# Performance work log

Hardware: AMD Instinct MI355X
Metric: run time of the kernel (lower is better)

Reference implementation:

```python
import jax, jax.numpy as jnp
import numpy as np

B, OBS, GENC, H, C, NF = 16384, 512, 216, 1024, 64, 8
IN = GENC + OBS + OBS  # use_state=True: [graph, state, next_state]


def setup_inputs() -> dict:
    key = jax.random.key(0)
    ks = jax.random.split(key, 9)
    graph = jax.random.randint(ks[0], (B, GENC), 0, 2).astype(jnp.float32)
    state = jax.random.normal(ks[1], (B, OBS), dtype=jnp.float32)
    next_state = jax.random.normal(ks[2], (B, OBS), dtype=jnp.float32)
    W1 = jax.random.normal(ks[3], (NF, IN, H), dtype=jnp.float32) * 0.02
    b1 = jnp.zeros((NF, H), dtype=jnp.float32)
    W2 = jax.random.normal(ks[4], (NF, H, H), dtype=jnp.float32) * 0.02
    b2 = jnp.zeros((NF, H), dtype=jnp.float32)
    W3 = jax.random.normal(ks[5], (NF, H, C), dtype=jnp.float32) * 0.02
    b3 = jnp.zeros((NF, C), dtype=jnp.float32)
    return {"graph": graph, "state": state, "next_state": next_state,
            "W1": W1, "b1": b1, "W2": W2, "b2": b2, "W3": W3, "b3": b3}


def reference(graph, state, next_state, W1, b1, W2, b2, W3, b3):
    # wide_diayn forward: concat input, run per-factor MLP on rows where
    # graph[:, i] == 1, later factors overwrite earlier; unmatched rows -> 0.
    x = jnp.concatenate([graph, state, next_state], axis=-1)  # [B, IN]
    nf = W1.shape[0]
    mask = graph[:, :nf] == 1.0  # [B, F] per-factor indicator
    h = jax.nn.relu(jnp.einsum('bi,fih->bfh', x, W1) + b1[None, :, :])
    h = jax.nn.relu(jnp.einsum('bfh,fhg->bfg', h, W2) + b2[None, :, :])
    out_all = jnp.einsum('bfg,fgc->bfc', h, W3) + b3[None, :, :]  # [B, F, C]
    rev_first = jnp.argmax(mask[:, ::-1].astype(jnp.int32), axis=1)
    last_idx = (nf - 1) - rev_first  # [B]
    sel = jnp.take_along_axis(out_all, last_idx[:, None, None], axis=1)[:, 0, :]
    any_active = mask.any(axis=1)
    return jnp.where(any_active[:, None], sel, jnp.zeros_like(sel))
```

## Files before the change

### kernel.cpp

```cpp
#include <hip/hip_runtime.h>

#define BB   16384
#define GENC 216
#define OBS  512
#define NH   1024
#define NC   64
#define NFAC 8
#define NIN  1240
#define KP1  1280
#define MTILES 136

typedef __attribute__((ext_vector_type(4))) float f32x4;
typedef __attribute__((ext_vector_type(8))) short short8;
typedef __attribute__((ext_vector_type(4))) short short4v;

__device__ __forceinline__ unsigned short f2bf(float f) {
  union { float f; unsigned u; } x; x.f = f;
  unsigned r = x.u + 0x7fffu + ((x.u >> 16) & 1u);
  return (unsigned short)(r >> 16);
}

__device__ __forceinline__ void gl_lds16(const unsigned short* g, unsigned short* l) {
  __builtin_amdgcn_global_load_lds(
      (const __attribute__((address_space(1))) void*)g,
      (__attribute__((address_space(3))) void*)l, 16, 0, 0);
}

__device__ __forceinline__ int xcd_chunk(int gid, int nwg) {
  int q = nwg >> 3, r = nwg & 7, x = gid & 7, p = gid >> 3;
  return (x < r ? x * (q + 1) : r * (q + 1) + (x - r) * q) + p;
}

__global__ void bucket_kernel(const float* __restrict__ graph,
                              int* __restrict__ cnt, int* __restrict__ rowlist) {
  __shared__ int lcnt[NFAC];
  __shared__ int lbase[NFAC];
  int tid = threadIdx.x;
  if (tid < NFAC) lcnt[tid] = 0;
  __syncthreads();
  int b = blockIdx.x * 256 + tid;
  const float* g = graph + (size_t)b * GENC;
  float4 g0 = *(const float4*)g;
  float4 g1 = *(const float4*)(g + 4);
  int f = -1;
  if (g0.x == 1.f) f = 0;
  if (g0.y == 1.f) f = 1;
  if (g0.z == 1.f) f = 2;
  if (g0.w == 1.f) f = 3;
  if (g1.x == 1.f) f = 4;
  if (g1.y == 1.f) f = 5;
  if (g1.z == 1.f) f = 6;
  if (g1.w == 1.f) f = 7;
  int li = 0;
  if (f >= 0) li = atomicAdd(&lcnt[f], 1);
  __syncthreads();
  if (tid < NFAC) lbase[tid] = lcnt[tid] ? atomicAdd(&cnt[tid], lcnt[tid]) : 0;
  __syncthreads();
  if (f >= 0) rowlist[f * BB + lbase[f] + li] = b;
}

__global__ void gather_x(const float* __restrict__ graph,
                         const float* __restrict__ state,
                         const float* __restrict__ nexts,
                         const int* __restrict__ cnt,
                         const int* __restrict__ rowlist,
                         unsigned short* __restrict__ xg) {
  int w = threadIdx.x >> 6, lane = threadIdx.x & 63;
  int pos = blockIdx.x * 4 + w;
  int f = -1, loc = 0, acc = 0;
#pragma unroll
  for (int i = 0; i < NFAC; ++i) {
    int c = cnt[i];
    if (f < 0 && pos < acc + c) { f = i; loc = pos - acc; }
    acc += c;
  }
  if (f < 0) return;
  int b = rowlist[f * BB + loc];
  unsigned short* dst = xg + (size_t)pos * KP1;
#pragma unroll
  for (int it = 0; it < 5; ++it) {
    int c = it * 64 + lane;
    float4 v;
    if (c < 54)       v = *(const float4*)(graph + (size_t)b * GENC + c * 4);
    else if (c < 182) v = *(const float4*)(state + (size_t)b * OBS + (c - 54) * 4);
    else if (c < 310) v = *(const float4*)(nexts + (size_t)b * OBS + (c - 182) * 4);
    else              v = make_float4(0.f, 0.f, 0.f, 0.f);
    short4v s;
    s[0] = (short)f2bf(v.x); s[1] = (short)f2bf(v.y);
    s[2] = (short)f2bf(v.z); s[3] = (short)f2bf(v.w);
    *(short4v*)(dst + c * 4) = s;
  }
}

__global__ void transpose_all(const float* __restrict__ W1,
                              const float* __restrict__ W2,
                              const float* __restrict__ W3,
                              unsigned short* __restrict__ w1t,
                              unsigned short* __restrict__ w2t,
                              unsigned short* __restrict__ w3t) {
  __shared__ unsigned short tile[64][65];
  int z = blockIdx.z;
  const float* src; unsigned short* dst; int K, N, KPad;
  if (z < 8)        { src = W1 + (size_t)z * NIN * NH;       dst = w1t + (size_t)z * NH * KP1; K = NIN; N = NH; KPad = KP1; }
  else if (z < 16)  { src = W2 + (size_t)(z - 8) * NH * NH;  dst = w2t + (size_t)(z - 8) * NH * NH; K = NH; N = NH; KPad = NH; }
  else              { src = W3 + (size_t)(z - 16) * NH * NC; dst = w3t + (size_t)(z - 16) * NC * NH; K = NH; N = NC; KPad = NH; }
  int k0 = blockIdx.y * 64, n0 = blockIdx.x * 64;
  if (k0 >= KPad || n0 >= N) return;
  int tr = threadIdx.x >> 6, tc = threadIdx.x & 63;
#pragma unroll
  for (int i = 0; i < 16; ++i) {
    int r = i * 4 + tr;
    int k = k0 + r;
    float v = (k < K) ? src[(size_t)k * N + n0 + tc] : 0.0f;
    tile[r][tc] = f2bf(v);
  }
  __syncthreads();
  int kp = threadIdx.x & 31, nb = threadIdx.x >> 5;
#pragma unroll
  for (int i = 0; i < 8; ++i) {
    int n = i * 8 + nb;
    union { short2 s2; unsigned u; } v;
    v.s2.x = (short)tile[kp * 2][n];
    v.s2.y = (short)tile[kp * 2 + 1][n];
    *(unsigned*)(dst + (size_t)(n0 + n) * KPad + k0 + kp * 2) = v.u;
  }
}

template <int LAYER>
__launch_bounds__(256, 2)
__global__ void mlp_gemm(const unsigned short* __restrict__ Abase,
                         const unsigned short* __restrict__ Wt,
                         const float* __restrict__ bias,
                         unsigned short* __restrict__ Hout,
                         float* __restrict__ Out,
                         const int* __restrict__ cnt,
                         const int* __restrict__ rowlist) {
  constexpr int N  = (LAYER == 3) ? NC : NH;
  constexpr int K  = (LAYER == 1) ? KP1 : NH;
  constexpr int BM = 128;
  constexpr int BN = (LAYER == 3) ? 64 : 128;
  constexpr int NB = (LAYER == 3) ? 1 : (NH / 128);
  constexpr int NKT = K / 64;
  constexpr int MF = (LAYER == 3) ? 2 : 4;
  constexpr int BI = (LAYER == 3) ? 2 : 4;

  const int wg = xcd_chunk(blockIdx.x, MTILES * NB);
  const int ty = wg / NB;
  const int n0 = (wg % NB) * BN;

  int f = -1, m0 = 0, goff = 0, cntf = 0;
  {
    int acc = 0, off = 0;
#pragma unroll
    for (int i = 0; i < NFAC; ++i) {
      int c = cnt[i];
      int t = (c + BM - 1) >> 7;
      if (f < 0 && ty < acc + t) { f = i; m0 = (ty - acc) * BM; goff = off; cntf = c; }
      acc += t; off += c;
    }
  }
  if (f < 0) return;

  __shared__ unsigned short As[2][BM * 64];
  __shared__ unsigned short Bs[2][BN * 64];

  const int tid = threadIdx.x;
  const int wid = tid >> 6, lane = tid & 63;
  const int wm = (LAYER == 3) ? wid : (wid >> 1);
  const int wn = (LAYER == 3) ? 0 : (wid & 1);

  const int rl = lane >> 3;
  const int chs = (lane & 7) ^ rl;
  const unsigned short* pA[4];
  const unsigned short* pB[BI];
  {
    const unsigned short* Aorg = Abase + (size_t)(goff + m0) * K;
    const unsigned short* Borg = Wt + (size_t)f * N * K + (size_t)n0 * K;
#pragma unroll
    for (int i = 0; i < 4; ++i)
      pA[i] = Aorg + (size_t)(wid * 32 + i * 8 + rl) * K + chs * 8;
#pragma unroll
    for (int i = 0; i < BI; ++i)
      pB[i] = Borg + (size_t)(wid * (8 * BI) + i * 8 + rl) * K + chs * 8;
  }

  f32x4 acc[MF][4];
#pragma unroll
  for (int a = 0; a < MF; ++a)
#pragma unroll
    for (int b = 0; b < 4; ++b) acc[a][b] = (f32x4){0.f, 0.f, 0.f, 0.f};

  auto stage = [&](int buf) {
#pragma unroll
    for (int i = 0; i < 4; ++i) {
      gl_lds16(pA[i], &As[buf][(wid * 32 + i * 8) * 64]);
      pA[i] += 64;
    }
#pragma unroll
    for (int i = 0; i < BI; ++i) {
      gl_lds16(pB[i], &Bs[buf][(wid * (8 * BI) + i * 8) * 64]);
      pB[i] += 64;
    }
  };

  auto compute = [&](int buf) {
#pragma unroll
    for (int ks = 0; ks < 2; ++ks) {
      const int kc8 = ks * 4 + (lane >> 4);
      short8 av[MF], bv[4];
#pragma unroll
      for (int mf = 0; mf < MF; ++mf) {
        int row = wm * (MF * 16) + mf * 16 + (lane & 15);
        av[mf] = *(const short8*)(&As[buf][0] + row * 64 + ((kc8 ^ (row & 7)) << 3));
      }
#pragma unroll
      for (int nf = 0; nf < 4; ++nf) {
        int col = wn * 64 + nf * 16 + (lane & 15);
        bv[nf] = *(const short8*)(&Bs[buf][0] + col * 64 + ((kc8 ^ (col & 7)) << 3));
      }
      __builtin_amdgcn_s_setprio(1);
#pragma unroll
      for (int mf = 0; mf < MF; ++mf)
#pragma unroll
        for (int nf = 0; nf < 4; ++nf)
          acc[mf][nf] = __builtin_amdgcn_mfma_f32_16x16x32_bf16(
              av[mf], bv[nf], acc[mf][nf], 0, 0, 0);
      __builtin_amdgcn_s_setprio(0);
    }
  };

  stage(0);
  stage(1);
#pragma unroll 1
  for (int kt = 0; kt < NKT; ++kt) {
    if (kt < NKT - 1) {
      if constexpr (LAYER == 3)
        asm volatile("s_waitcnt vmcnt(6)" ::: "memory");
      else
        asm volatile("s_waitcnt vmcnt(8)" ::: "memory");
    } else {
      asm volatile("s_waitcnt vmcnt(0)" ::: "memory");
    }
    __builtin_amdgcn_sched_barrier(0);
    __builtin_amdgcn_s_barrier();
    __builtin_amdgcn_sched_barrier(0);
    compute(kt & 1);
    __builtin_amdgcn_sched_barrier(0);
    __builtin_amdgcn_s_barrier();
    __builtin_amdgcn_sched_barrier(0);
    if (kt + 2 < NKT) stage(kt & 1);
  }

  if (LAYER == 3) {
    const float* bs = bias + f * NC;
#pragma unroll
    for (int nf = 0; nf < 4; ++nf) {
      int col = nf * 16 + (lane & 15);
      float bv = bs[col];
#pragma unroll
      for (int mf = 0; mf < MF; ++mf) {
        int rbase = wm * (MF * 16) + mf * 16 + ((lane >> 4) << 2);
#pragma unroll
        for (int i = 0; i < 4; ++i) {
          int pos = m0 + rbase + i;
          if (pos < cntf) {
            int b = rowlist[f * BB + pos];
            Out[(size_t)b * NC + col] = acc[mf][nf][i] + bv;
          }
        }
      }
    }
  } else {
    const float* bs = bias + f * NH;
#pragma unroll
    for (int nf = 0; nf < 4; ++nf) {
      int col = n0 + wn * 64 + nf * 16 + (lane & 15);
      float bv = bs[col];
#pragma unroll
      for (int mf = 0; mf < MF; ++mf) {
        int rbase = wm * (MF * 16) + mf * 16 + ((lane >> 4) << 2);
#pragma unroll
        for (int i = 0; i < 4; ++i) {
          int pos = m0 + rbase + i;
          if (pos < cntf) {
            float v = fmaxf(acc[mf][nf][i] + bv, 0.0f);
            Hout[(size_t)(goff + pos) * NH + col] = f2bf(v);
          }
        }
      }
    }
  }
}

extern "C" void kernel_launch(void* const* d_in, const int* in_sizes, int n_in,
                              void* d_out, int out_size, void* d_ws, size_t ws_size,
                              hipStream_t stream) {
  const float* graph = (const float*)d_in[0];
  const float* state = (const float*)d_in[1];
  const float* nexts = (const float*)d_in[2];
  const float* W1 = (const float*)d_in[3];
  const float* b1 = (const float*)d_in[4];
  const float* W2 = (const float*)d_in[5];
  const float* b2 = (const float*)d_in[6];
  const float* W3 = (const float*)d_in[7];
  const float* b3 = (const float*)d_in[8];
  float* out = (float*)d_out;
  char* ws = (char*)d_ws;

  const size_t ROWCAP = BB + 128;
  const size_t OFF_ROW = 256;
  const size_t OFF_W1T = OFF_ROW + (size_t)NFAC * BB * 4;
  const size_t OFF_W2T = OFF_W1T + (size_t)NFAC * NH * KP1 * 2;
  const size_t OFF_W3T = OFF_W2T + (size_t)NFAC * NH * NH * 2;
  const size_t OFF_H1  = OFF_W3T + (size_t)NFAC * NC * NH * 2;
  const size_t OFF_XG  = OFF_H1 + ROWCAP * NH * 2;

  int* cnt = (int*)ws;
  int* rowlist = (int*)(ws + OFF_ROW);
  unsigned short* w1t = (unsigned short*)(ws + OFF_W1T);
  unsigned short* w2t = (unsigned short*)(ws + OFF_W2T);
  unsigned short* w3t = (unsigned short*)(ws + OFF_W3T);
  unsigned short* h1  = (unsigned short*)(ws + OFF_H1);
  unsigned short* xg  = (unsigned short*)(ws + OFF_XG);
  unsigned short* h2  = xg;

  hipMemsetAsync(cnt, 0, 64, stream);
  hipMemsetAsync(d_out, 0, (size_t)out_size * sizeof(float), stream);

  bucket_kernel<<<BB / 256, 256, 0, stream>>>(graph, cnt, rowlist);
  gather_x<<<BB / 4, 256, 0, stream>>>(graph, state, nexts, cnt, rowlist, xg);
  transpose_all<<<dim3(16, 20, 24), 256, 0, stream>>>(W1, W2, W3, w1t, w2t, w3t);

  mlp_gemm<1><<<MTILES * (NH / 128), 256, 0, stream>>>(
      xg, w1t, b1, h1, nullptr, cnt, rowlist);
  mlp_gemm<2><<<MTILES * (NH / 128), 256, 0, stream>>>(
      h1, w2t, b2, h2, nullptr, cnt, rowlist);
  mlp_gemm<3><<<MTILES, 256, 0, stream>>>(
      h2, w3t, b3, nullptr, out, cnt, rowlist);
}
```

Before: 254.0 us.

## Merge prep kernels, use single-buffer K=128 tiles for layers 1-2, split layer-3 kernel

Fuses the input gather and weight transpose into one launch. Layers 1 and 2 now stage a 128-deep K tile into a single LDS buffer per iteration with plain __syncthreads, replacing the double-buffered 64-deep pipeline with vmcnt waits and setprio. Layer 3 gets its own kernel with 64-row tiles, giving more workgroups. The single-buffer GEMM loop gives up load/compute overlap in exchange for fewer barriers per K and larger tiles.

```diff
diff --git a/kernel.cpp b/kernel.cpp
--- a/kernel.cpp
+++ b/kernel.cpp
@@ -9,6 +9,7 @@
 #define NIN  1240
 #define KP1  1280
 #define MTILES 136
+#define MT64  264
 
 typedef __attribute__((ext_vector_type(4))) float f32x4;
 typedef __attribute__((ext_vector_type(8))) short short8;
@@ -59,70 +60,73 @@
   if (f >= 0) rowlist[f * BB + lbase[f] + li] = b;
 }
 
-__global__ void gather_x(const float* __restrict__ graph,
-                         const float* __restrict__ state,
-                         const float* __restrict__ nexts,
-                         const int* __restrict__ cnt,
-                         const int* __restrict__ rowlist,
-                         unsigned short* __restrict__ xg) {
-  int w = threadIdx.x >> 6, lane = threadIdx.x & 63;
-  int pos = blockIdx.x * 4 + w;
-  int f = -1, loc = 0, acc = 0;
-#pragma unroll
-  for (int i = 0; i < NFAC; ++i) {
-    int c = cnt[i];
-    if (f < 0 && pos < acc + c) { f = i; loc = pos - acc; }
-    acc += c;
-  }
-  if (f < 0) return;
-  int b = rowlist[f * BB + loc];
-  unsigned short* dst = xg + (size_t)pos * KP1;
-#pragma unroll
-  for (int it = 0; it < 5; ++it) {
-    int c = it * 64 + lane;
-    float4 v;
-    if (c < 54)       v = *(const float4*)(graph + (size_t)b * GENC + c * 4);
-    else if (c < 182) v = *(const float4*)(state + (size_t)b * OBS + (c - 54) * 4);
-    else if (c < 310) v = *(const float4*)(nexts + (size_t)b * OBS + (c - 182) * 4);
-    else              v = make_float4(0.f, 0.f, 0.f, 0.f);
-    short4v s;
-    s[0] = (short)f2bf(v.x); s[1] = (short)f2bf(v.y);
-    s[2] = (short)f2bf(v.z); s[3] = (short)f2bf(v.w);
-    *(short4v*)(dst + c * 4) = s;
-  }
-}
-
-__global__ void transpose_all(const float* __restrict__ W1,
-                              const float* __restrict__ W2,
-                              const float* __restrict__ W3,
-                              unsigned short* __restrict__ w1t,
-                              unsigned short* __restrict__ w2t,
-                              unsigned short* __restrict__ w3t) {
+__global__ void prep_kernel(const float* __restrict__ graph,
+                            const float* __restrict__ state,
+                            const float* __restrict__ nexts,
+                            const int* __restrict__ cnt,
+                            const int* __restrict__ rowlist,
+                            unsigned short* __restrict__ xg,
+                            const float* __restrict__ W1,
+                            const float* __restrict__ W2,
+                            const float* __restrict__ W3,
+                            unsigned short* __restrict__ w1t,
+                            unsigned short* __restrict__ w2t,
+                            unsigned short* __restrict__ w3t) {
   __shared__ unsigned short tile[64][65];
-  int z = blockIdx.z;
-  const float* src; unsigned short* dst; int K, N, KPad;
-  if (z < 8)        { src = W1 + (size_t)z * NIN * NH;       dst = w1t + (size_t)z * NH * KP1; K = NIN; N = NH; KPad = KP1; }
-  else if (z < 16)  { src = W2 + (size_t)(z - 8) * NH * NH;  dst = w2t + (size_t)(z - 8) * NH * NH; K = NH; N = NH; KPad = NH; }
-  else              { src = W3 + (size_t)(z - 16) * NH * NC; dst = w3t + (size_t)(z - 16) * NC * NH; K = NH; N = NC; KPad = NH; }
-  int k0 = blockIdx.y * 64, n0 = blockIdx.x * 64;
-  if (k0 >= KPad || n0 >= N) return;
-  int tr = threadIdx.x >> 6, tc = threadIdx.x & 63;
-#pragma unroll
-  for (int i = 0; i < 16; ++i) {
-    int r = i * 4 + tr;
-    int k = k0 + r;
-    float v = (k < K) ? src[(size_t)k * N + n0 + tc] : 0.0f;
-    tile[r][tc] = f2bf(v);
-  }
-  __syncthreads();
-  int kp = threadIdx.x & 31, nb = threadIdx.x >> 5;
-#pragma unroll
-  for (int i = 0; i < 8; ++i) {
-    int n = i * 8 + nb;
-    union { short2 s2; unsigned u; } v;
-    v.s2.x = (short)tile[kp * 2][n];
-    v.s2.y = (short)tile[kp * 2 + 1][n];
-    *(unsigned*)(dst + (size_t)(n0 + n) * KPad + k0 + kp * 2) = v.u;
+  const int blk = blockIdx.x;
+  if (blk < 4096) {
+    int w = threadIdx.x >> 6, lane = threadIdx.x & 63;
+    int pos = blk * 4 + w;
+    int f = -1, loc = 0, acc = 0;
+#pragma unroll
+    for (int i = 0; i < NFAC; ++i) {
+      int c = cnt[i];
+      if (f < 0 && pos < acc + c) { f = i; loc = pos - acc; }
+      acc += c;
+    }
+    if (f < 0) return;
+    int b = rowlist[f * BB + loc];
+    unsigned short* dst = xg + (size_t)pos * KP1;
+#pragma unroll
+    for (int it = 0; it < 5; ++it) {
+      int c = it * 64 + lane;
+      float4 v;
+      if (c < 54)       v = *(const float4*)(graph + (size_t)b * GENC + c * 4);
+      else if (c < 182) v = *(const float4*)(state + (size_t)b * OBS + (c - 54) * 4);
+      else if (c < 310) v = *(const float4*)(nexts + (size_t)b * OBS + (c - 182) * 4);
+      else              v = make_float4(0.f, 0.f, 0.f, 0.f);
+      short4v s;
+      s[0] = (short)f2bf(v.x); s[1] = (short)f2bf(v.y);
+      s[2] = (short)f2bf(v.z); s[3] = (short)f2bf(v.w);
+      *(short4v*)(dst + c * 4) = s;
+    }
+  } else {
+    int t = blk - 4096;
+    int x = t & 15, y = (t >> 4) % 20, z = t / 320;
+    const float* src; unsigned short* dst; int K, N, KPad;
+    if (z < 8)        { src = W1 + (size_t)z * NIN * NH;       dst = w1t + (size_t)z * NH * KP1;       K = NIN; N = NH; KPad = KP1; }
+    else if (z < 16)  { src = W2 + (size_t)(z - 8) * NH * NH;  dst = w2t + (size_t)(z - 8) * NH * NH;  K = NH;  N = NH; KPad = NH; }
+    else              { src = W3 + (size_t)(z - 16) * NH * NC; dst = w3t + (size_t)(z - 16) * NC * NH; K = NH;  N = NC; KPad = NH; }
+    int k0 = y * 64, n0 = x * 64;
+    if (k0 >= KPad || n0 >= N) return;
+    int tr = threadIdx.x >> 6, tc = threadIdx.x & 63;
+#pragma unroll
+    for (int i = 0; i < 16; ++i) {
+      int r = i * 4 + tr;
+      int k = k0 + r;
+      float v = (k < K) ? src[(size_t)k * N + n0 + tc] : 0.0f;
+      tile[r][tc] = f2bf(v);
+    }
+    __syncthreads();
+    int kp = threadIdx.x & 31, nb = threadIdx.x >> 5;
+#pragma unroll
+    for (int i = 0; i < 8; ++i) {
+      int n = i * 8 + nb;
+      union { short2 s2; unsigned u; } v;
+      v.s2.x = (short)tile[kp * 2][n];
+      v.s2.y = (short)tile[kp * 2 + 1][n];
+      *(unsigned*)(dst + (size_t)(n0 + n) * KPad + k0 + kp * 2) = v.u;
+    }
   }
 }
 
@@ -132,21 +136,14 @@
                          const unsigned short* __restrict__ Wt,
                          const float* __restrict__ bias,
                          unsigned short* __restrict__ Hout,
-                         float* __restrict__ Out,
-                         const int* __restrict__ cnt,
-                         const int* __restrict__ rowlist) {
-  constexpr int N  = (LAYER == 3) ? NC : NH;
-  constexpr int K  = (LAYER == 1) ? KP1 : NH;
-  constexpr int BM = 128;
-  constexpr int BN = (LAYER == 3) ? 64 : 128;
-  constexpr int NB = (LAYER == 3) ? 1 : (NH / 128);
-  constexpr int NKT = K / 64;
-  constexpr int MF = (LAYER == 3) ? 2 : 4;
-  constexpr int BI = (LAYER == 3) ? 2 : 4;
+                         const int* __restrict__ cnt) {
+  constexpr int K   = (LAYER == 1) ? KP1 : NH;
+  constexpr int NKT = K / 128;
+  constexpr int NB  = NH / 128;
 
   const int wg = xcd_chunk(blockIdx.x, MTILES * NB);
   const int ty = wg / NB;
-  const int n0 = (wg % NB) * BN;
+  const int n0 = (wg % NB) * 128;
 
   int f = -1, m0 = 0, goff = 0, cntf = 0;
   {
@@ -154,78 +151,146 @@
 #pragma unroll
     for (int i = 0; i < NFAC; ++i) {
       int c = cnt[i];
-      int t = (c + BM - 1) >> 7;
-      if (f < 0 && ty < acc + t) { f = i; m0 = (ty - acc) * BM; goff = off; cntf = c; }
+      int t = (c + 127) >> 7;
+      if (f < 0 && ty < acc + t) { f = i; m0 = (ty - acc) * 128; goff = off; cntf = c; }
       acc += t; off += c;
     }
   }
   if (f < 0) return;
 
-  __shared__ unsigned short As[2][BM * 64];
-  __shared__ unsigned short Bs[2][BN * 64];
-
-  const int tid = threadIdx.x;
-  const int wid = tid >> 6, lane = tid & 63;
-  const int wm = (LAYER == 3) ? wid : (wid >> 1);
-  const int wn = (LAYER == 3) ? 0 : (wid & 1);
-
-  const int rl = lane >> 3;
-  const int chs = (lane & 7) ^ rl;
-  const unsigned short* pA[4];
-  const unsigned short* pB[BI];
-  {
-    const unsigned short* Aorg = Abase + (size_t)(goff + m0) * K;
-    const unsigned short* Borg = Wt + (size_t)f * N * K + (size_t)n0 * K;
-#pragma unroll
-    for (int i = 0; i < 4; ++i)
-      pA[i] = Aorg + (size_t)(wid * 32 + i * 8 + rl) * K + chs * 8;
-#pragma unroll
-    for (int i = 0; i < BI; ++i)
-      pB[i] = Borg + (size_t)(wid * (8 * BI) + i * 8 + rl) * K + chs * 8;
-  }
-
-  f32x4 acc[MF][4];
-#pragma unroll
-  for (int a = 0; a < MF; ++a)
+  __shared__ unsigned short As[128 * 128];
+  __shared__ unsigned short Bs[128 * 128];
+
+  const int tid = threadIdx.x, wid = tid >> 6, lane = tid & 63;
+  const int wm = wid >> 1, wn = wid & 1;
+
+  const int sr = tid >> 4;
+  const int chs = (tid & 15) ^ sr;
+  const unsigned short* pa = Abase + (size_t)(goff + m0 + sr) * K + chs * 8;
+  const unsigned short* pb = Wt + (size_t)f * NH * K + (size_t)(n0 + sr) * K + chs * 8;
+
+  f32x4 acc[4][4];
+#pragma unroll
+  for (int a = 0; a < 4; ++a)
 #pragma unroll
     for (int b = 0; b < 4; ++b) acc[a][b] = (f32x4){0.f, 0.f, 0.f, 0.f};
 
-  auto stage = [&](int buf) {
-#pragma unroll
-    for (int i = 0; i < 4; ++i) {
-      gl_lds16(pA[i], &As[buf][(wid * 32 + i * 8) * 64]);
-      pA[i] += 64;
-    }
-#pragma unroll
-    for (int i = 0; i < BI; ++i) {
-      gl_lds16(pB[i], &Bs[buf][(wid * (8 * BI) + i * 8) * 64]);
-      pB[i] += 64;
-    }
-  };
-
-  auto compute = [&](int buf) {
-#pragma unroll
-    for (int ks = 0; ks < 2; ++ks) {
-      const int kc8 = ks * 4 + (lane >> 4);
-      short8 av[MF], bv[4];
-#pragma unroll
-      for (int mf = 0; mf < MF; ++mf) {
-        int row = wm * (MF * 16) + mf * 16 + (lane & 15);
-        av[mf] = *(const short8*)(&As[buf][0] + row * 64 + ((kc8 ^ (row & 7)) << 3));
+  for (int kt = 0; kt < NKT; ++kt) {
+#pragma unroll
+    for (int i = 0; i < 8; ++i)
+      gl_lds16(pa + (size_t)i * 16 * K, As + i * 2048 + tid * 8);
+#pragma unroll
+    for (int i = 0; i < 8; ++i)
+      gl_lds16(pb + (size_t)i * 16 * K, Bs + i * 2048 + tid * 8);
+    pa += 128; pb += 128;
+    __syncthreads();
+#pragma unroll
+    for (int ks = 0; ks < 4; ++ks) {
+      const int kc = ks * 4 + (lane >> 4);
+      short8 av[4], bv[4];
+#pragma unroll
+      for (int mf = 0; mf < 4; ++mf) {
+        int row = wm * 64 + mf * 16 + (lane & 15);
+        av[mf] = *(const short8*)(As + row * 128 + ((kc ^ (row & 15)) << 3));
       }
 #pragma unroll
       for (int nf = 0; nf < 4; ++nf) {
         int col = wn * 64 + nf * 16 + (lane & 15);
-        bv[nf] = *(const short8*)(&Bs[buf][0] + col * 64 + ((kc8 ^ (col & 7)) << 3));
-      }
-      __builtin_amdgcn_s_setprio(1);
-#pragma unroll
-      for (int mf = 0; mf < MF; ++mf)
+        bv[nf] = *(const short8*)(Bs + col * 128 + ((kc ^ (col & 15)) << 3));
+      }
+#pragma unroll
+      for (int mf = 0; mf < 4; ++mf)
 #pragma unroll
         for (int nf = 0; nf < 4; ++nf)
           acc[mf][nf] = __builtin_amdgcn_mfma_f32_16x16x32_bf16(
               av[mf], bv[nf], acc[mf][nf], 0, 0, 0);
-      __builtin_amdgcn_s_setprio(0);
+    }
+    __syncthreads();
+  }
+
+  const float* bs = bias + f * NH;
+#pragma unroll
+  for (int nf = 0; nf < 4; ++nf) {
+    int col = n0 + wn * 64 + nf * 16 + (lane & 15);
+    float bvv = bs[col];
+#pragma unroll
+    for (int mf = 0; mf < 4; ++mf) {
+      int rbase = wm * 64 + mf * 16 + ((lane >> 4) << 2);
+#pragma unroll
+      for (int i = 0; i < 4; ++i) {
+        int pos = m0 + rbase + i;
+        if (pos < cntf) {
+          float v = fmaxf(acc[mf][nf][i] + bvv, 0.0f);
+          Hout[(size_t)(goff + pos) * NH + col] = f2bf(v);
+        }
+      }
+    }
+  }
+}
+
+__launch_bounds__(256, 2)
+__global__ void mlp_gemm3(const unsigned short* __restrict__ Abase,
+                          const unsigned short* __restrict__ Wt,
+                          const float* __restrict__ bias,
+                          float* __restrict__ Out,
+                          const int* __restrict__ cnt,
+                          const int* __restrict__ rowlist) {
+  constexpr int K = NH;
+  constexpr int NKT = K / 64;
+
+  const int ty = xcd_chunk(blockIdx.x, MT64);
+
+  int f = -1, m0 = 0, goff = 0, cntf = 0;
+  {
+    int acc = 0, off = 0;
+#pragma unroll
+    for (int i = 0; i < NFAC; ++i) {
+      int c = cnt[i];
+      int t = (c + 63) >> 6;
+      if (f < 0 && ty < acc + t) { f = i; m0 = (ty - acc) * 64; goff = off; cntf = c; }
+      acc += t; off += c;
+    }
+  }
+  if (f < 0) return;
+
+  __shared__ unsigned short As[2][64 * 64];
+  __shared__ unsigned short Bs[2][64 * 64];
+
+  const int tid = threadIdx.x;
+  const int wid = tid >> 6, lane = tid & 63;
+
+  const int sr = tid >> 3;
+  const int chs = (tid & 7) ^ (sr & 7);
+  const unsigned short* pA = Abase + (size_t)(goff + m0 + sr) * K + chs * 8;
+  const unsigned short* pB = Wt + (size_t)f * NC * K + (size_t)sr * K + chs * 8;
+
+  f32x4 acc[4];
+#pragma unroll
+  for (int b = 0; b < 4; ++b) acc[b] = (f32x4){0.f, 0.f, 0.f, 0.f};
+
+  auto stage = [&](int buf) {
+#pragma unroll
+    for (int i = 0; i < 2; ++i) gl_lds16(pA + (size_t)i * 32 * K, &As[buf][i * 2048 + tid * 8]);
+#pragma unroll
+    for (int i = 0; i < 2; ++i) gl_lds16(pB + (size_t)i * 32 * K, &Bs[buf][i * 2048 + tid * 8]);
+    pA += 64; pB += 64;
+  };
+
+  auto compute = [&](int buf) {
+#pragma unroll
+    for (int ks = 0; ks < 2; ++ks) {
+      const int kc = ks * 4 + (lane >> 4);
+      int row = wid * 16 + (lane & 15);
+      short8 av = *(const short8*)(&As[buf][0] + row * 64 + ((kc ^ (row & 7)) << 3));
+      short8 bv[4];
+#pragma unroll
+      for (int nf = 0; nf < 4; ++nf) {
+        int col = nf * 16 + (lane & 15);
+        bv[nf] = *(const short8*)(&Bs[buf][0] + col * 64 + ((kc ^ (col & 7)) << 3));
+      }
+#pragma unroll
+      for (int nf = 0; nf < 4; ++nf)
+        acc[nf] = __builtin_amdgcn_mfma_f32_16x16x32_bf16(av, bv[nf], acc[nf], 0, 0, 0);
     }
   };
 
@@ -233,14 +298,8 @@
   stage(1);
 #pragma unroll 1
   for (int kt = 0; kt < NKT; ++kt) {
-    if (kt < NKT - 1) {
-      if constexpr (LAYER == 3)
-        asm volatile("s_waitcnt vmcnt(6)" ::: "memory");
-      else
-        asm volatile("s_waitcnt vmcnt(8)" ::: "memory");
-    } else {
-      asm volatile("s_waitcnt vmcnt(0)" ::: "memory");
-    }
+    if (kt < NKT - 1) { asm volatile("s_waitcnt vmcnt(4)" ::: "memory"); }
+    else              { asm volatile("s_waitcnt vmcnt(0)" ::: "memory"); }
     __builtin_amdgcn_sched_barrier(0);
     __builtin_amdgcn_s_barrier();
     __builtin_amdgcn_sched_barrier(0);
@@ -251,42 +310,18 @@
     if (kt + 2 < NKT) stage(kt & 1);
   }
 
-  if (LAYER == 3) {
-    const float* bs = bias + f * NC;
-#pragma unroll
-    for (int nf = 0; nf < 4; ++nf) {
-      int col = nf * 16 + (lane & 15);
-      float bv = bs[col];
-#pragma unroll
-      for (int mf = 0; mf < MF; ++mf) {
-        int rbase = wm * (MF * 16) + mf * 16 + ((lane >> 4) << 2);
-#pragma unroll
-        for (int i = 0; i < 4; ++i) {
-          int pos = m0 + rbase + i;
-          if (pos < cntf) {
-            int b = rowlist[f * BB + pos];
-            Out[(size_t)b * NC + col] = acc[mf][nf][i] + bv;
-          }
-        }
-      }
-    }
-  } else {
-    const float* bs = bias + f * NH;
-#pragma unroll
-    for (int nf = 0; nf < 4; ++nf) {
-      int col = n0 + wn * 64 + nf * 16 + (lane & 15);
-      float bv = bs[col];
-#pragma unroll
-      for (int mf = 0; mf < MF; ++mf) {
-        int rbase = wm * (MF * 16) + mf * 16 + ((lane >> 4) << 2);
-#pragma unroll
-        for (int i = 0; i < 4; ++i) {
-          int pos = m0 + rbase + i;
-          if (pos < cntf) {
-            float v = fmaxf(acc[mf][nf][i] + bv, 0.0f);
-            Hout[(size_t)(goff + pos) * NH + col] = f2bf(v);
-          }
-        }
+  const float* bs = bias + f * NC;
+#pragma unroll
+  for (int nf = 0; nf < 4; ++nf) {
+    int col = nf * 16 + (lane & 15);
+    float bvv = bs[col];
+    int rbase = wid * 16 + ((lane >> 4) << 2);
+#pragma unroll
+    for (int i = 0; i < 4; ++i) {
+      int pos = m0 + rbase + i;
+      if (pos < cntf) {
+        int b = rowlist[f * BB + pos];
+        Out[(size_t)b * NC + col] = acc[nf][i] + bvv;
       }
     }
   }
@@ -307,7 +342,7 @@
   float* out = (float*)d_out;
   char* ws = (char*)d_ws;
 
-  const size_t ROWCAP = BB + 128;
+  const size_t ROWCAP = BB + 256;
   const size_t OFF_ROW = 256;
   const size_t OFF_W1T = OFF_ROW + (size_t)NFAC * BB * 4;
   const size_t OFF_W2T = OFF_W1T + (size_t)NFAC * NH * KP1 * 2;
@@ -328,13 +363,10 @@
   hipMemsetAsync(d_out, 0, (size_t)out_size * sizeof(float), stream);
 
   bucket_kernel<<<BB / 256, 256, 0, stream>>>(graph, cnt, rowlist);
-  gather_x<<<BB / 4, 256, 0, stream>>>(graph, state, nexts, cnt, rowlist, xg);
-  transpose_all<<<dim3(16, 20, 24), 256, 0, stream>>>(W1, W2, W3, w1t, w2t, w3t);
-
-  mlp_gemm<1><<<MTILES * (NH / 128), 256, 0, stream>>>(
-      xg, w1t, b1, h1, nullptr, cnt, rowlist);
-  mlp_gemm<2><<<MTILES * (NH / 128), 256, 0, stream>>>(
-      h1, w2t, b2, h2, nullptr, cnt, rowlist);
-  mlp_gemm<3><<<MTILES, 256, 0, stream>>>(
-      h2, w3t, b3, nullptr, out, cnt, rowlist);
-}
+  prep_kernel<<<4096 + 7680, 256, 0, stream>>>(graph, state, nexts, cnt, rowlist,
+                                               xg, W1, W2, W3, w1t, w2t, w3t);
+
+  mlp_gemm<1><<<MTILES * 8, 256, 0, stream>>>(xg, w1t, b1, h1, cnt);
+  mlp_gemm<2><<<MTILES * 8, 256, 0, stream>>>(h1, w2t, b2, h2, cnt);
+  mlp_gemm3<<<MT64, 256, 0, stream>>>(h2, w3t, b3, out, cnt, rowlist);
+}
```

After: 237.1 us. 1.07x faster.
